# Optimization experiments

Measured on AMD Instinct MI355X. Metric: run time of the kernel, lower is better.

## Reference

```python
import jax, jax.numpy as jnp
import numpy as np

HEADS = 8
HID = 256
D = HID // HEADS
NEG_SLOPE = 0.2  # PyG leaky_relu negative_slope default in HANConv
NA, NPAP, CIN = 10000, 20000, 256
E = 256000
OUT = 16


def seg_softmax(scores, seg, num_segments):
    # scores: [E, H]; softmax over edges sharing the same dst segment id
    m = jax.ops.segment_max(scores, seg, num_segments=num_segments)
    m = jnp.where(jnp.isfinite(m), m, 0.0)
    e = jnp.exp(scores - m[seg])
    s = jax.ops.segment_sum(e, seg, num_segments=num_segments)
    return e / (s[seg] + 1e-16)


def han_edge(h_src, h_dst, att_src, att_dst, src, dst, num_dst):
    # h_src: [Ns, H, D]; att_*: [H, D]; src/dst: [E]
    a = (h_src * att_src).sum(-1)[src] + (h_dst * att_dst).sum(-1)[dst]  # [E, H]
    alpha = seg_softmax(jax.nn.leaky_relu(a, NEG_SLOPE), dst, num_dst)
    out = jax.ops.segment_sum(h_src[src] * alpha[..., None], dst, num_segments=num_dst)
    return jax.nn.relu(out.reshape(num_dst, HID))


def semantic_group(xs, q, k_W, k_b):
    out = jnp.stack(xs)                                            # [M, N, F]
    score = (jnp.tanh(out @ k_W + k_b) * q).sum(-1).mean(axis=1)   # [M]
    attn = jax.nn.softmax(score)                                   # softmax over metapaths
    return (out * attn[:, None, None]).sum(0)                      # [N, F]


def setup_inputs() -> dict:
    key = jax.random.key(0)
    ks = jax.random.split(key, 32)
    n = lambda i, shape, s: jax.random.normal(ks[i], shape, dtype=jnp.float32) * s
    ri = lambda i, hi: jax.random.randint(ks[i], (E,), 0, hi).astype(jnp.int64)
    w_scale = (1.0 / CIN) ** 0.5
    return {
        "x_author": n(0, (NA, CIN), 1.0),
        "x_paper": n(1, (NPAP, CIN), 1.0),
        "W_author": n(2, (CIN, HID), w_scale),
        "b_author": jnp.zeros((HID,), jnp.float32),
        "W_paper": n(3, (CIN, HID), w_scale),
        "b_paper": jnp.zeros((HID,), jnp.float32),
        "att_sw": n(4, (HEADS, D), 0.1),
        "att_dw": n(5, (HEADS, D), 0.1),
        "att_sc": n(6, (HEADS, D), 0.1),
        "att_dc": n(7, (HEADS, D), 0.1),
        "att_sr": n(8, (HEADS, D), 0.1),
        "att_dr": n(9, (HEADS, D), 0.1),
        "k_W": n(10, (HID, HID), (1.0 / HID) ** 0.5),
        "k_b": jnp.zeros((HID,), jnp.float32),
        "q": n(11, (HID,), 0.1),
        "lin_W": n(12, (HID, OUT), (1.0 / HID) ** 0.5),
        "lin_b": jnp.zeros((OUT,), jnp.float32),
        "ew_src": ri(13, NA), "ew_dst": ri(14, NPAP),
        "ec_src": ri(15, NPAP), "ec_dst": ri(16, NPAP),
        "er_src": ri(17, NPAP), "er_dst": ri(18, NA),
    }


def reference(x_author, x_paper, W_author, b_author, W_paper, b_paper,
              att_sw, att_dw, att_sc, att_dc, att_sr, att_dr,
              k_W, k_b, q, lin_W, lin_b,
              ew_src, ew_dst, ec_src, ec_dst, er_src, er_dst):
    # per-node-type projection -> [N, H, D]
    h_a = (x_author @ W_author + b_author).reshape(NA, HEADS, D)
    h_p = (x_paper @ W_paper + b_paper).reshape(NPAP, HEADS, D)
    # per-edge-type gather / attention / segment-softmax / scatter
    o_writes = han_edge(h_a, h_p, att_sw, att_dw, ew_src, ew_dst, NPAP)  # author->paper
    o_cites = han_edge(h_p, h_p, att_sc, att_dc, ec_src, ec_dst, NPAP)   # paper->paper
    o_rev = han_edge(h_p, h_a, att_sr, att_dr, er_src, er_dst, NA)       # paper->author
    # semantic-level attention over metapaths per dst node type
    paper_out = semantic_group([o_writes, o_cites], q, k_W, k_b)
    author_out = semantic_group([o_rev], q, k_W, k_b)
    # global_add_pool per node type (batch=None -> single graph) + shared linear
    pooled = jnp.stack([author_out.sum(0), paper_out.sum(0)])  # [2, HID]
    return pooled @ lin_W + lin_b                              # [2, OUT]
```

## Files before the change

### kernel.cpp

```cpp
#include <hip/hip_runtime.h>
#include <hip/hip_bf16.h>

#define HEADS 8
#define HID 256
#define NA 10000
#define NPAP 20000
#define NE 256000
#define N_SEG (2 * NPAP + NA)
#define TOTE (3 * NE)
#define NEG_SLOPE 0.2f
#define NBA 157
#define NBP 313
#define PROJ_BLKS (4 * (NBA + NBP))
#define DEG_BLKS 3000
#define NATT_BLKS (NPAP + NA)
#define NBS ((N_SEG + 255) / 256)

typedef __attribute__((ext_vector_type(8))) short bf16x8;
typedef __attribute__((ext_vector_type(4))) float f32x4;

__device__ __forceinline__ short f2bf(float x) {
    unsigned u = __float_as_uint(x);
    unsigned r = (u + 0x7fffu + ((u >> 16) & 1u)) >> 16;
    return (short)r;
}
__device__ __forceinline__ float bf2f(short s) {
    return __uint_as_float(((unsigned)(unsigned short)s) << 16);
}

__global__ __launch_bounds__(256) void wconv(
    const float* __restrict__ W_a, short* __restrict__ WaT,
    const float* __restrict__ W_p, short* __restrict__ WpT,
    const float* __restrict__ k_W, short* __restrict__ kWT)
{
    __shared__ short T[64][65];
    int b = blockIdx.x;
    int t = threadIdx.x;
    int z = b >> 4, rem = b & 15;
    int k0 = (rem & 3) * 64, c0 = (rem >> 2) * 64;
    const float* W = z == 0 ? W_a : (z == 1 ? W_p : k_W);
    short* Wt      = z == 0 ? WaT : (z == 1 ? WpT : kWT);
    int rr = t >> 6, c = t & 63;
#pragma unroll
    for (int p = 0; p < 16; ++p) {
        int r = rr + p * 4;
        T[c][r] = f2bf(W[(size_t)(k0 + r) * 256 + c0 + c]);
    }
    __syncthreads();
#pragma unroll
    for (int p = 0; p < 16; ++p) {
        int cc = rr + p * 4;
        Wt[(size_t)(c0 + cc) * 256 + k0 + c] = T[cc][c];
    }
}

__global__ __launch_bounds__(256) void proj_deg(
    const float* __restrict__ A0, const short* __restrict__ Wt0, const float* __restrict__ b0,
    short* __restrict__ C0, unsigned char* __restrict__ H80,
    const float* __restrict__ A1, const short* __restrict__ Wt1, const float* __restrict__ b1,
    short* __restrict__ C1, unsigned char* __restrict__ H81,
    const int* __restrict__ ewd, const int* __restrict__ ecd, const int* __restrict__ erd,
    int* __restrict__ deg4, unsigned short* __restrict__ rank16)
{
    __shared__ short As[64][64];
    __shared__ short Ws2[64][64];

    int b = blockIdx.x;
    int t = threadIdx.x;

    if (b >= PROJ_BLKS) {
        int bb = b - PROJ_BLKS;
        int e = bb * 256 + t;
        if (e >= TOTE) return;
        int d;
        if (e < NE)          d = ewd[e];
        else if (e < 2 * NE) d = ecd[e - NE] + NPAP;
        else                 d = erd[e - 2 * NE] + 2 * NPAP;
        int r = atomicAdd(&deg4[(bb & 3) * N_SEG + d], 1);
        rank16[e] = (unsigned short)r;
        return;
    }

    const float* A; const short* Wt; const float* bias; short* Cb; unsigned char* H8; int N, row0, col0;
    if (b < 4 * NBA) { A = A0; Wt = Wt0; bias = b0; Cb = C0; H8 = H80; N = NA;
                       row0 = (b >> 2) * 64; col0 = (b & 3) * 64; }
    else             { int bb = b - 4 * NBA;
                       A = A1; Wt = Wt1; bias = b1; Cb = C1; H8 = H81; N = NPAP;
                       row0 = (bb >> 2) * 64; col0 = (bb & 3) * 64; }

    int w = t >> 6, l = t & 63;
    int lr = l & 15, lh = l >> 4;
    int swz = (l & 7) << 3;

    f32x4 acc[4] = {};

    for (int k0 = 0; k0 < 256; k0 += 64) {
#pragma unroll
        for (int i = 0; i < 4; ++i) {
            int lin = t + i * 256;
            int r = lin >> 4, fc = (lin & 15) << 2;
            float4 v = make_float4(0.f, 0.f, 0.f, 0.f);
            int gr = row0 + r;
            if (gr < N) v = *reinterpret_cast<const float4*>(&A[(size_t)gr * 256 + k0 + fc]);
            short4 o;
            o.x = f2bf(v.x); o.y = f2bf(v.y); o.z = f2bf(v.z); o.w = f2bf(v.w);
            *reinterpret_cast<short4*>(&As[r][fc ^ ((r & 7) << 3)]) = o;
        }
#pragma unroll
        for (int i = 0; i < 2; ++i) {
            int lin = t + i * 256;
            int c = lin >> 3, kc = (lin & 7) << 3;
            *reinterpret_cast<bf16x8*>(&Ws2[c][kc ^ ((c & 7) << 3)]) =
                *reinterpret_cast<const bf16x8*>(&Wt[(size_t)(col0 + c) * 256 + k0 + kc]);
        }
        __syncthreads();
#pragma unroll
        for (int kk = 0; kk < 64; kk += 32) {
            int krow = (kk + lh * 8) ^ swz;
            bf16x8 af = *reinterpret_cast<bf16x8*>(&As[w * 16 + lr][krow]);
            bf16x8 bfr[4];
#pragma unroll
            for (int ni = 0; ni < 4; ++ni)
                bfr[ni] = *reinterpret_cast<bf16x8*>(&Ws2[ni * 16 + lr][krow]);
#pragma unroll
            for (int ni = 0; ni < 4; ++ni)
                acc[ni] = __builtin_amdgcn_mfma_f32_16x16x32_bf16(af, bfr[ni], acc[ni], 0, 0, 0);
        }
        __syncthreads();
    }

    int rb = row0 + w * 16 + lh * 4;
#pragma unroll
    for (int ni = 0; ni < 4; ++ni) {
        int c = col0 + ni * 16 + lr;
        float bc = bias[c];
#pragma unroll
        for (int j = 0; j < 4; ++j) {
            if (rb + j < N) {
                float v = acc[ni][j] + bc;
                Cb[(size_t)(rb + j) * 256 + c] = f2bf(v);
                unsigned pk = __builtin_amdgcn_cvt_pk_fp8_f32(v, v, 0, false);
                H8[(size_t)(rb + j) * 256 + c] = (unsigned char)pk;
            }
        }
    }
}

__global__ __launch_bounds__(256) void natt_scan(
    const short* __restrict__ h_p, const short* __restrict__ h_a,
    const float* __restrict__ att_dw, const float* __restrict__ att_sc,
    const float* __restrict__ att_dc, const float* __restrict__ att_sr,
    const float* __restrict__ att_sw, const float* __restrict__ att_dr,
    float* __restrict__ a_dw, float* __restrict__ a_sc,
    float* __restrict__ a_dc, float* __restrict__ a_sr,
    float* __restrict__ a_sw, float* __restrict__ a_dr,
    const int* __restrict__ deg4, int* __restrict__ excl, int* __restrict__ bsum)
{
    int b = blockIdx.x;
    int t = threadIdx.x;

    if (b >= NATT_BLKS) {
        __shared__ int buf[256];
        int bb = b - NATT_BLKS;
        int idx = bb * 256 + t;
        int v = 0;
        if (idx < N_SEG)
            v = deg4[idx] + deg4[N_SEG + idx] + deg4[2 * N_SEG + idx] + deg4[3 * N_SEG + idx];
        buf[t] = v;
        __syncthreads();
        for (int off = 1; off < 256; off <<= 1) {
            int add = (t >= off) ? buf[t - off] : 0;
            __syncthreads();
            buf[t] += add;
            __syncthreads();
        }
        if (idx < N_SEG) excl[idx] = buf[t] - v;
        if (t == 255) bsum[bb] = buf[255];
        return;
    }

    if (b < NPAP) {
        float v = bf2f(h_p[(size_t)b * 256 + t]);
        float d0 = v * att_dw[t], d1 = v * att_sc[t], d2 = v * att_dc[t], d3 = v * att_sr[t];
#pragma unroll
        for (int k = 16; k > 0; k >>= 1) {
            d0 += __shfl_xor(d0, k, 64);
            d1 += __shfl_xor(d1, k, 64);
            d2 += __shfl_xor(d2, k, 64);
            d3 += __shfl_xor(d3, k, 64);
        }
        if ((t & 31) == 0) {
            int hh = t >> 5;
            a_dw[b * 8 + hh] = d0; a_sc[b * 8 + hh] = d1;
            a_dc[b * 8 + hh] = d2; a_sr[b * 8 + hh] = d3;
        }
    } else {
        int m = b - NPAP;
        float v = bf2f(h_a[(size_t)m * 256 + t]);
        float d0 = v * att_sw[t], d1 = v * att_dr[t];
#pragma unroll
        for (int k = 16; k > 0; k >>= 1) {
            d0 += __shfl_xor(d0, k, 64);
            d1 += __shfl_xor(d1, k, 64);
        }
        if ((t & 31) == 0) {
            int hh = t >> 5;
            a_sw[m * 8 + hh] = d0; a_dr[m * 8 + hh] = d1;
        }
    }
}

__global__ void scan_l2(const int* __restrict__ bsum, int* __restrict__ boff, int nb)
{
    __shared__ int buf[256];
    int t = threadIdx.x;
    int v = (t < nb) ? bsum[t] : 0;
    buf[t] = v;
    __syncthreads();
    for (int off = 1; off < 256; off <<= 1) {
        int add = (t >= off) ? buf[t - off] : 0;
        __syncthreads();
        buf[t] += add;
        __syncthreads();
    }
    if (t < nb) boff[t] = buf[t] - v;
}

__global__ void scan_l3(const int* __restrict__ excl, const int* __restrict__ boff,
                        const int* __restrict__ deg4,
                        int* __restrict__ starts, int* __restrict__ base4, int N)
{
    int i = blockIdx.x * 256 + threadIdx.x;
    if (i > N) return;
    int v = (i == N) ? TOTE : excl[i] + boff[i >> 8];
    starts[i] = v;
    if (i < N) {
        int c = v;
        base4[i] = c;                 c += deg4[i];
        base4[N_SEG + i] = c;         c += deg4[N_SEG + i];
        base4[2 * N_SEG + i] = c;     c += deg4[2 * N_SEG + i];
        base4[3 * N_SEG + i] = c;
    }
}

__global__ __launch_bounds__(256) void scatter_edges(
    const int* __restrict__ ews, const int* __restrict__ ewd,
    const int* __restrict__ ecs, const int* __restrict__ ecd,
    const int* __restrict__ ers, const int* __restrict__ erd,
    const int* __restrict__ base4, const unsigned short* __restrict__ rank16,
    int* __restrict__ ssrc)
{
    int e = blockIdx.x * 256 + threadIdx.x;
    if (e >= TOTE) return;
    int s, d;
    if (e < NE)          { s = ews[e];          d = ewd[e]; }
    else if (e < 2 * NE) { s = ecs[e - NE];     d = ecd[e - NE] + NPAP; }
    else                 { s = ers[e - 2 * NE]; d = erd[e - 2 * NE] + 2 * NPAP; }
    int shadow = (e >> 8) & 3;
    int pos = base4[shadow * N_SEG + d] + (int)rank16[e];
    ssrc[pos] = s;
}

__global__ __launch_bounds__(256) void han_seg(
    const int* __restrict__ starts, const int* __restrict__ ssrc,
    const float* __restrict__ a_sw, const float* __restrict__ a_dw,
    const float* __restrict__ a_sc, const float* __restrict__ a_dc,
    const float* __restrict__ a_sr, const float* __restrict__ a_dr,
    const unsigned* __restrict__ h8_a, const unsigned* __restrict__ h8_p,
    short* __restrict__ outall)
{
    int w = threadIdx.x >> 6, lane = threadIdx.x & 63;
    int n = blockIdx.x * 4 + w;
    if (n >= N_SEG) return;

    const float* asrc; const float* adst; const unsigned* h8;
    int nloc;
    if (n < NPAP)          { nloc = n;            asrc = a_sw; adst = a_dw; h8 = h8_a; }
    else if (n < 2 * NPAP) { nloc = n - NPAP;     asrc = a_sc; adst = a_dc; h8 = h8_p; }
    else                   { nloc = n - 2 * NPAP; asrc = a_sr; adst = a_dr; h8 = h8_p; }

    int hh = lane >> 3;
    int c0 = lane << 2;
    float ad = adst[nloc * 8 + hh];

    int i = starts[n], end = starts[n + 1];
    float ac0 = 0.f, ac1 = 0.f, ac2 = 0.f, ac3 = 0.f, ps = 0.f;

    for (; i + 4 <= end; i += 4) {
        int s0 = __builtin_amdgcn_readfirstlane(ssrc[i]);
        int s1 = __builtin_amdgcn_readfirstlane(ssrc[i + 1]);
        int s2 = __builtin_amdgcn_readfirstlane(ssrc[i + 2]);
        int s3 = __builtin_amdgcn_readfirstlane(ssrc[i + 3]);
        float x0 = asrc[s0 * 8 + hh] + ad;
        float x1 = asrc[s1 * 8 + hh] + ad;
        float x2 = asrc[s2 * 8 + hh] + ad;
        float x3 = asrc[s3 * 8 + hh] + ad;
        unsigned v0 = h8[s0 * 64 + lane];
        unsigned v1 = h8[s1 * 64 + lane];
        unsigned v2 = h8[s2 * 64 + lane];
        unsigned v3 = h8[s3 * 64 + lane];
        x0 = x0 > 0.f ? x0 : NEG_SLOPE * x0;
        x1 = x1 > 0.f ? x1 : NEG_SLOPE * x1;
        x2 = x2 > 0.f ? x2 : NEG_SLOPE * x2;
        x3 = x3 > 0.f ? x3 : NEG_SLOPE * x3;
        float e0 = __expf(x0), e1 = __expf(x1), e2 = __expf(x2), e3 = __expf(x3);
        ps += (e0 + e1) + (e2 + e3);
        ac0 += e0 * __builtin_amdgcn_cvt_f32_fp8(v0, 0) + e1 * __builtin_amdgcn_cvt_f32_fp8(v1, 0)
             + e2 * __builtin_amdgcn_cvt_f32_fp8(v2, 0) + e3 * __builtin_amdgcn_cvt_f32_fp8(v3, 0);
        ac1 += e0 * __builtin_amdgcn_cvt_f32_fp8(v0, 1) + e1 * __builtin_amdgcn_cvt_f32_fp8(v1, 1)
             + e2 * __builtin_amdgcn_cvt_f32_fp8(v2, 1) + e3 * __builtin_amdgcn_cvt_f32_fp8(v3, 1);
        ac2 += e0 * __builtin_amdgcn_cvt_f32_fp8(v0, 2) + e1 * __builtin_amdgcn_cvt_f32_fp8(v1, 2)
             + e2 * __builtin_amdgcn_cvt_f32_fp8(v2, 2) + e3 * __builtin_amdgcn_cvt_f32_fp8(v3, 2);
        ac3 += e0 * __builtin_amdgcn_cvt_f32_fp8(v0, 3) + e1 * __builtin_amdgcn_cvt_f32_fp8(v1, 3)
             + e2 * __builtin_amdgcn_cvt_f32_fp8(v2, 3) + e3 * __builtin_amdgcn_cvt_f32_fp8(v3, 3);
    }
    for (; i < end; ++i) {
        int s0 = __builtin_amdgcn_readfirstlane(ssrc[i]);
        float x0 = asrc[s0 * 8 + hh] + ad;
        unsigned v0 = h8[s0 * 64 + lane];
        x0 = x0 > 0.f ? x0 : NEG_SLOPE * x0;
        float e0 = __expf(x0);
        ps += e0;
        ac0 += e0 * __builtin_amdgcn_cvt_f32_fp8(v0, 0);
        ac1 += e0 * __builtin_amdgcn_cvt_f32_fp8(v0, 1);
        ac2 += e0 * __builtin_amdgcn_cvt_f32_fp8(v0, 2);
        ac3 += e0 * __builtin_amdgcn_cvt_f32_fp8(v0, 3);
    }

    float inv = 1.0f / (ps + 1e-16f);
    float o0 = ac0 * inv, o1 = ac1 * inv, o2 = ac2 * inv, o3 = ac3 * inv;
    short4 o;
    o.x = f2bf(o0 > 0.f ? o0 : 0.f);
    o.y = f2bf(o1 > 0.f ? o1 : 0.f);
    o.z = f2bf(o2 > 0.f ? o2 : 0.f);
    o.w = f2bf(o3 > 0.f ? o3 : 0.f);
    *reinterpret_cast<short4*>(&outall[(size_t)n * 256 + c0]) = o;
}

__global__ void colsum3(const short* __restrict__ outall,
                        float* __restrict__ cw, float* __restrict__ cc,
                        float* __restrict__ cr)
{
    int t = threadIdx.x;
    int r0 = blockIdx.x * 32;
    int rend = r0 + 32 < N_SEG ? r0 + 32 : N_SEG;
    float s = 0.f;
    for (int r = r0; r < rend; ++r) s += bf2f(outall[(size_t)r * 256 + t]);
    float* cs = r0 < NPAP ? cw : (r0 < 2 * NPAP ? cc : cr);
    atomicAdd(&cs[t], s);
}

__global__ __launch_bounds__(256) void gemm_score(
    const short* __restrict__ A0, const short* __restrict__ Wt, const float* __restrict__ kb,
    float* __restrict__ sAcc0, int N0, int nb0,
    const short* __restrict__ A1, float* __restrict__ sAcc1, int N1,
    const float* __restrict__ q)
{
    __shared__ short As[64][64];
    __shared__ short Ws[256][64];
    __shared__ float red[256];

    int bx = blockIdx.x;
    const short* A; float* sAcc; int N, row0;
    if (bx < nb0) { A = A0; sAcc = sAcc0; N = N0; row0 = bx * 64; }
    else          { A = A1; sAcc = sAcc1; N = N1; row0 = (bx - nb0) * 64; }

    int tid = threadIdx.x;
    int w = tid >> 6, l = tid & 63;
    int lr = l & 15, lh = l >> 4;
    int swz = (l & 7) << 3;

    f32x4 acc[4][4] = {};

    for (int k0 = 0; k0 < 256; k0 += 64) {
#pragma unroll
        for (int i = 0; i < 2; ++i) {
            int lin = tid + i * 256;
            int r = lin >> 3, kc = (lin & 7) << 3;
            bf16x8 v = {};
            int gr = row0 + r;
            if (gr < N) v = *reinterpret_cast<const bf16x8*>(&A[(size_t)gr * 256 + k0 + kc]);
            *reinterpret_cast<bf16x8*>(&As[r][kc ^ ((r & 7) << 3)]) = v;
        }
#pragma unroll
        for (int i = 0; i < 8; ++i) {
            int lin = tid + i * 256;
            int c = lin >> 3, kc = (lin & 7) << 3;
            *reinterpret_cast<bf16x8*>(&Ws[c][kc ^ ((c & 7) << 3)]) =
                *reinterpret_cast<const bf16x8*>(&Wt[(size_t)c * 256 + k0 + kc]);
        }
        __syncthreads();
#pragma unroll
        for (int kk = 0; kk < 64; kk += 32) {
            int krow = (kk + lh * 8) ^ swz;
            bf16x8 af[4], bfr[4];
#pragma unroll
            for (int mi = 0; mi < 4; ++mi)
                af[mi] = *reinterpret_cast<bf16x8*>(&As[mi * 16 + lr][krow]);
#pragma unroll
            for (int ni = 0; ni < 4; ++ni)
                bfr[ni] = *reinterpret_cast<bf16x8*>(&Ws[w * 64 + ni * 16 + lr][krow]);
#pragma unroll
            for (int mi = 0; mi < 4; ++mi)
#pragma unroll
                for (int ni = 0; ni < 4; ++ni)
                    acc[mi][ni] = __builtin_amdgcn_mfma_f32_16x16x32_bf16(
                        af[mi], bfr[ni], acc[mi][ni], 0, 0, 0);
        }
        __syncthreads();
    }

    float s = 0.f;
#pragma unroll
    for (int mi = 0; mi < 4; ++mi) {
        int rb = row0 + mi * 16 + lh * 4;
#pragma unroll
        for (int ni = 0; ni < 4; ++ni) {
            int c = w * 64 + ni * 16 + lr;
            float bc = kb[c], qc = q[c];
#pragma unroll
            for (int j = 0; j < 4; ++j) {
                if (rb + j < N) s += tanhf(acc[mi][ni][j] + bc) * qc;
            }
        }
    }
    red[tid] = s;
    __syncthreads();
    for (int k = 128; k > 0; k >>= 1) {
        if (tid < k) red[tid] += red[tid + k];
        __syncthreads();
    }
    if (tid == 0) atomicAdd(sAcc, red[0]);
}

__global__ void finalize(const float* __restrict__ scoreAcc,
                         const float* __restrict__ colsum_w, const float* __restrict__ colsum_c,
                         const float* __restrict__ colsum_r,
                         const float* __restrict__ lin_W, const float* __restrict__ lin_b,
                         float* __restrict__ out)
{
    int t = threadIdx.x;
    if (t >= 32) return;
    float sw = scoreAcc[0] / (float)NPAP;
    float scs = scoreAcc[1] / (float)NPAP;
    float mx = fmaxf(sw, scs);
    float ew = expf(sw - mx), ec = expf(scs - mx);
    float aw = ew / (ew + ec), ac = ec / (ew + ec);
    int row = t >> 4, j = t & 15;
    float acc = lin_b[j];
    for (int c = 0; c < 256; ++c) {
        float p = (row == 0) ? colsum_r[c] : (aw * colsum_w[c] + ac * colsum_c[c]);
        acc += p * lin_W[c * 16 + j];
    }
    out[row * 16 + j] = acc;
}

extern "C" void kernel_launch(void* const* d_in, const int* in_sizes, int n_in,
                              void* d_out, int out_size, void* d_ws, size_t ws_size,
                              hipStream_t stream)
{
    const float* x_a   = (const float*)d_in[0];
    const float* x_p   = (const float*)d_in[1];
    const float* W_a   = (const float*)d_in[2];
    const float* b_a   = (const float*)d_in[3];
    const float* W_p   = (const float*)d_in[4];
    const float* b_p   = (const float*)d_in[5];
    const float* att_sw = (const float*)d_in[6];
    const float* att_dw = (const float*)d_in[7];
    const float* att_sc = (const float*)d_in[8];
    const float* att_dc = (const float*)d_in[9];
    const float* att_sr = (const float*)d_in[10];
    const float* att_dr = (const float*)d_in[11];
    const float* k_W   = (const float*)d_in[12];
    const float* k_b   = (const float*)d_in[13];
    const float* q     = (const float*)d_in[14];
    const float* lin_W = (const float*)d_in[15];
    const float* lin_b = (const float*)d_in[16];
    const int* ew_src = (const int*)d_in[17];
    const int* ew_dst = (const int*)d_in[18];
    const int* ec_src = (const int*)d_in[19];
    const int* ec_dst = (const int*)d_in[20];
    const int* er_src = (const int*)d_in[21];
    const int* er_dst = (const int*)d_in[22];

    float* ws = (float*)d_ws;
    size_t off = 0;
    auto align4 = [&]() { off = (off + 3) & ~(size_t)3; };

    short* h_a_bf = (short*)(ws + off); off += (size_t)NA * HID / 2;
    short* h_p_bf = (short*)(ws + off); off += (size_t)NPAP * HID / 2;
    unsigned char* h8_a = (unsigned char*)(ws + off); off += (size_t)NA * HID / 4;
    unsigned char* h8_p = (unsigned char*)(ws + off); off += (size_t)NPAP * HID / 4;
    short* WaT  = (short*)(ws + off); off += 256 * 256 / 2;
    short* WpT  = (short*)(ws + off); off += 256 * 256 / 2;
    short* kWT  = (short*)(ws + off); off += 256 * 256 / 2;
    float* a_sw = ws + off; off += (size_t)NA * 8;
    float* a_dw = ws + off; off += (size_t)NPAP * 8;
    float* a_sc = ws + off; off += (size_t)NPAP * 8;
    float* a_dc = ws + off; off += (size_t)NPAP * 8;
    float* a_sr = ws + off; off += (size_t)NPAP * 8;
    float* a_dr = ws + off; off += (size_t)NA * 8;
    short* outall = (short*)(ws + off); off += (size_t)N_SEG * HID / 2;
    int* starts  = (int*)(ws + off); off += N_SEG + 1; align4();
    int* base4   = (int*)(ws + off); off += 4 * N_SEG; align4();
    int* sexcl   = (int*)(ws + off); off += N_SEG + 1; align4();
    int* sbsum   = (int*)(ws + off); off += 256;
    int* sboff   = (int*)(ws + off); off += 256;
    int* ssrc    = (int*)(ws + off); off += TOTE;
    unsigned short* rank16 = (unsigned short*)(ws + off); off += TOTE / 2;
    size_t zero_start = off;
    int* deg4       = (int*)(ws + off); off += 4 * N_SEG; align4();
    float* colsum_w = ws + off; off += 256;
    float* colsum_c = ws + off; off += 256;
    float* colsum_r = ws + off; off += 256;
    float* score    = ws + off; off += 2;
    size_t zero_bytes = (off - zero_start) * sizeof(float);

    hipMemsetAsync(ws + zero_start, 0, zero_bytes, stream);

    wconv<<<48, 256, 0, stream>>>(W_a, WaT, W_p, WpT, k_W, kWT);

    proj_deg<<<PROJ_BLKS + DEG_BLKS, 256, 0, stream>>>(
        x_a, WaT, b_a, h_a_bf, h8_a,
        x_p, WpT, b_p, h_p_bf, h8_p,
        ew_dst, ec_dst, er_dst, deg4, rank16);

    natt_scan<<<NATT_BLKS + NBS, 256, 0, stream>>>(
        h_p_bf, h_a_bf, att_dw, att_sc, att_dc, att_sr, att_sw, att_dr,
        a_dw, a_sc, a_dc, a_sr, a_sw, a_dr,
        deg4, sexcl, sbsum);

    scan_l2<<<1, 256, 0, stream>>>(sbsum, sboff, NBS);
    scan_l3<<<(N_SEG + 1 + 255) / 256, 256, 0, stream>>>(sexcl, sboff, deg4, starts, base4, N_SEG);

    scatter_edges<<<(TOTE + 255) / 256, 256, 0, stream>>>(ew_src, ew_dst, ec_src, ec_dst,
                                                          er_src, er_dst, base4, rank16, ssrc);

    han_seg<<<(N_SEG + 3) / 4, 256, 0, stream>>>(starts, ssrc, a_sw, a_dw, a_sc, a_dc, a_sr, a_dr,
                                                 (const unsigned*)h8_a, (const unsigned*)h8_p,
                                                 outall);

    colsum3<<<(N_SEG + 31) / 32, 256, 0, stream>>>(outall, colsum_w, colsum_c, colsum_r);
    gemm_score<<<2 * NBP, 256, 0, stream>>>(
        outall, kWT, k_b, score + 0, NPAP, NBP,
        outall + (size_t)NPAP * HID, score + 1, NPAP, q);

    finalize<<<1, 64, 0, stream>>>(score, colsum_w, colsum_c, colsum_r, lin_W, lin_b, (float*)d_out);
}
```

Measured before the change: 245.8 us.

## Compute full 256-column output tile per block in projection GEMM

The projection GEMM now assigns each block a 64-row by 256-column tile instead of a 64x64 tile, with each wave handling 64 columns and 4x4 MFMA accumulators. Each A row tile is loaded and converted from fp32 to bf16 once rather than four times, which removes redundant global reads of the activations. The cost is four times fewer projection blocks, a larger shared-memory W tile (32 KB), and higher register pressure from 16 accumulators, so occupancy and latency hiding may suffer.

```diff
diff --git a/kernel.cpp b/kernel.cpp
--- a/kernel.cpp
+++ b/kernel.cpp
@@ -11,7 +11,7 @@
 #define NEG_SLOPE 0.2f
 #define NBA 157
 #define NBP 313
-#define PROJ_BLKS (4 * (NBA + NBP))
+#define PROJ_BLKS (NBA + NBP)
 #define DEG_BLKS 3000
 #define NATT_BLKS (NPAP + NA)
 #define NBS ((N_SEG + 255) / 256)
@@ -63,7 +63,7 @@
     int* __restrict__ deg4, unsigned short* __restrict__ rank16)
 {
     __shared__ short As[64][64];
-    __shared__ short Ws2[64][64];
+    __shared__ short Ws[256][64];
 
     int b = blockIdx.x;
     int t = threadIdx.x;
@@ -81,18 +81,15 @@
         return;
     }
 
-    const float* A; const short* Wt; const float* bias; short* Cb; unsigned char* H8; int N, row0, col0;
-    if (b < 4 * NBA) { A = A0; Wt = Wt0; bias = b0; Cb = C0; H8 = H80; N = NA;
-                       row0 = (b >> 2) * 64; col0 = (b & 3) * 64; }
-    else             { int bb = b - 4 * NBA;
-                       A = A1; Wt = Wt1; bias = b1; Cb = C1; H8 = H81; N = NPAP;
-                       row0 = (bb >> 2) * 64; col0 = (bb & 3) * 64; }
+    const float* A; const short* Wt; const float* bias; short* Cb; unsigned char* H8; int N, row0;
+    if (b < NBA) { A = A0; Wt = Wt0; bias = b0; Cb = C0; H8 = H80; N = NA;   row0 = b * 64; }
+    else         { A = A1; Wt = Wt1; bias = b1; Cb = C1; H8 = H81; N = NPAP; row0 = (b - NBA) * 64; }
 
     int w = t >> 6, l = t & 63;
     int lr = l & 15, lh = l >> 4;
     int swz = (l & 7) << 3;
 
-    f32x4 acc[4] = {};
+    f32x4 acc[4][4] = {};
 
     for (int k0 = 0; k0 < 256; k0 += 64) {
 #pragma unroll
@@ -107,40 +104,48 @@
             *reinterpret_cast<short4*>(&As[r][fc ^ ((r & 7) << 3)]) = o;
         }
 #pragma unroll
-        for (int i = 0; i < 2; ++i) {
+        for (int i = 0; i < 8; ++i) {
             int lin = t + i * 256;
             int c = lin >> 3, kc = (lin & 7) << 3;
-            *reinterpret_cast<bf16x8*>(&Ws2[c][kc ^ ((c & 7) << 3)]) =
-                *reinterpret_cast<const bf16x8*>(&Wt[(size_t)(col0 + c) * 256 + k0 + kc]);
+            *reinterpret_cast<bf16x8*>(&Ws[c][kc ^ ((c & 7) << 3)]) =
+                *reinterpret_cast<const bf16x8*>(&Wt[(size_t)c * 256 + k0 + kc]);
         }
         __syncthreads();
 #pragma unroll
         for (int kk = 0; kk < 64; kk += 32) {
             int krow = (kk + lh * 8) ^ swz;
-            bf16x8 af = *reinterpret_cast<bf16x8*>(&As[w * 16 + lr][krow]);
-            bf16x8 bfr[4];
+            bf16x8 af[4], bfr[4];
+#pragma unroll
+            for (int mi = 0; mi < 4; ++mi)
+                af[mi] = *reinterpret_cast<bf16x8*>(&As[mi * 16 + lr][krow]);
 #pragma unroll
             for (int ni = 0; ni < 4; ++ni)
-                bfr[ni] = *reinterpret_cast<bf16x8*>(&Ws2[ni * 16 + lr][krow]);
-#pragma unroll
-            for (int ni = 0; ni < 4; ++ni)
-                acc[ni] = __builtin_amdgcn_mfma_f32_16x16x32_bf16(af, bfr[ni], acc[ni], 0, 0, 0);
-        }
-        __syncthreads();
-    }
-
-    int rb = row0 + w * 16 + lh * 4;
-#pragma unroll
-    for (int ni = 0; ni < 4; ++ni) {
-        int c = col0 + ni * 16 + lr;
-        float bc = bias[c];
-#pragma unroll
-        for (int j = 0; j < 4; ++j) {
-            if (rb + j < N) {
-                float v = acc[ni][j] + bc;
-                Cb[(size_t)(rb + j) * 256 + c] = f2bf(v);
-                unsigned pk = __builtin_amdgcn_cvt_pk_fp8_f32(v, v, 0, false);
-                H8[(size_t)(rb + j) * 256 + c] = (unsigned char)pk;
+                bfr[ni] = *reinterpret_cast<bf16x8*>(&Ws[w * 64 + ni * 16 + lr][krow]);
+#pragma unroll
+            for (int mi = 0; mi < 4; ++mi)
+#pragma unroll
+                for (int ni = 0; ni < 4; ++ni)
+                    acc[mi][ni] = __builtin_amdgcn_mfma_f32_16x16x32_bf16(
+                        af[mi], bfr[ni], acc[mi][ni], 0, 0, 0);
+        }
+        __syncthreads();
+    }
+
+#pragma unroll
+    for (int mi = 0; mi < 4; ++mi) {
+        int rb = row0 + mi * 16 + lh * 4;
+#pragma unroll
+        for (int ni = 0; ni < 4; ++ni) {
+            int c = w * 64 + ni * 16 + lr;
+            float bc = bias[c];
+#pragma unroll
+            for (int j = 0; j < 4; ++j) {
+                if (rb + j < N) {
+                    float v = acc[mi][ni][j] + bc;
+                    Cb[(size_t)(rb + j) * 256 + c] = f2bf(v);
+                    unsigned pk = __builtin_amdgcn_cvt_pk_fp8_f32(v, v, 0, false);
+                    H8[(size_t)(rb + j) * 256 + c] = (unsigned char)pk;
+                }
             }
         }
     }
```

After: 230.4 us (median of 3 runs). -6.3%, faster.
